# Performance work log

Hardware: AMD Instinct MI355X
Metric: run time of the kernel (lower is better)

Reference implementation:

```python
import jax, jax.numpy as jnp
import numpy as np

DIM = 1024
EXPAND = 2
HEAD_DIM = 64
D_STATE = 128
N_GROUPS = 1
D_CONV = 4
D_INNER = DIM * EXPAND            # 2048
N_HEADS = D_INNER // HEAD_DIM     # 32
CONV_DIM = D_INNER + 2 * N_GROUPS * D_STATE  # 2304
D_IN_PROJ = 2 * D_INNER + 2 * N_GROUPS * D_STATE + N_HEADS  # 4384
SEQLEN = 4096
LN_EPS = 1e-5


def setup_inputs() -> dict:
    key = jax.random.key(0)
    ks = jax.random.split(key, 6)
    x = jax.random.normal(ks[0], (SEQLEN, DIM), dtype=jnp.float32)
    W_in = jax.random.normal(ks[1], (D_IN_PROJ, DIM), dtype=jnp.float32) * 0.02
    conv_w = jax.random.normal(ks[2], (CONV_DIM, 1, D_CONV), dtype=jnp.float32) * 0.2
    conv_b = jax.random.normal(ks[3], (CONV_DIM,), dtype=jnp.float32) * 0.02
    # dt_bias init per module: dt ~ exp(U*(log(dt_max)-log(dt_min))+log(dt_min)); inv-softplus
    u = jax.random.uniform(ks[4], (N_HEADS,))
    dt = jnp.exp(u * (np.log(0.1) - np.log(0.001)) + np.log(0.001))
    dt = jnp.clip(dt, 1e-4)
    dt_bias = dt + jnp.log(-jnp.expm1(-dt))
    A_log = jnp.log(jax.random.uniform(ks[5], (N_HEADS,), minval=1.0, maxval=16.0))
    D = jnp.ones((N_HEADS,), dtype=jnp.float32)
    ln_w = jnp.ones((D_INNER,), dtype=jnp.float32)
    ln_b = jnp.zeros((D_INNER,), dtype=jnp.float32)
    W_out = jax.random.normal(jax.random.fold_in(key, 7), (DIM, D_INNER), dtype=jnp.float32) * 0.02
    return {"x": x, "W_in": W_in, "conv_w": conv_w, "conv_b": conv_b,
            "dt_bias": dt_bias, "A_log": A_log, "D": D,
            "ln_w": ln_w, "ln_b": ln_b, "W_out": W_out}


def _forward(x, W_in, conv_w, conv_b, dt_bias, A_log, D, ln_w, ln_b, W_out):
    L = x.shape[0]
    dtype = x.dtype
    A = -jnp.exp(A_log.astype(jnp.float32))  # (h,)
    zxbcdt = x @ W_in.T                       # (L, d_in_proj)
    z = zxbcdt[:, :D_INNER]                   # (L, d_inner)
    xbc = zxbcdt[:, D_INNER:D_INNER + CONV_DIM]
    dt = zxbcdt[:, -N_HEADS:]
    dt = jax.nn.softplus(dt.astype(jnp.float32) + dt_bias.astype(jnp.float32))  # (L, h)
    # depthwise 1D conv, SAME padding (module uses padding='SAME', then slices to L)
    xbc_c = jax.lax.conv_general_dilated(
        xbc.T[None],                          # (1, conv_dim, L)
        conv_w,                               # (conv_dim, 1, k)
        window_strides=(1,), padding='SAME',
        dimension_numbers=('NCH', 'OIH', 'NCH'),
        feature_group_count=CONV_DIM,
    )[0].T + conv_b                           # (L, conv_dim)
    xbc_s = jax.nn.silu(xbc_c)
    x_in = xbc_s[:, :D_INNER].reshape(L, N_HEADS, HEAD_DIM)      # (L, h, p)
    B = xbc_s[:, D_INNER:D_INNER + N_GROUPS * D_STATE]          # (L, n) with g=1
    C = xbc_s[:, D_INNER + N_GROUPS * D_STATE:]                 # (L, n)
    # non-causal linear attention (VSSD): y = C (B^T (x * dt * A)) + x * D
    dA = dt.astype(dtype) * A.astype(dtype)                     # (L, h)
    Vs = x_in * dA[..., None]                                   # (L, h, p)
    KV = jnp.einsum('ln,lhp->hnp', B, Vs)                       # (h, n, p)
    y = jnp.einsum('ln,hnp->lhp', C, KV) + x_in * D[None, :, None]
    y = y.reshape(L, D_INNER)
    # per-token LayerNorm, then multiplicative SiLU(z) gate
    mu = jnp.mean(y, axis=-1, keepdims=True)
    var = jnp.var(y, axis=-1, keepdims=True)
    yn = (y - mu) * jax.lax.rsqrt(var + LN_EPS) * ln_w + ln_b
    y = yn * jax.nn.silu(z)
    return y @ W_out.T                                          # (L, dim)


def reference(x, W_in, conv_w, conv_b, dt_bias, A_log, D, ln_w, ln_b, W_out):
    return _forward(x, W_in, conv_w, conv_b, dt_bias, A_log, D, ln_w, ln_b, W_out)
```

## Files before the change

kernel.cpp:

```cpp
#include <hip/hip_runtime.h>
#include <math.h>

#define SEQLEN    4096
#define DIM_IN    1024
#define D_INNER   2048
#define N_HEADS   32
#define D_STATE   128
#define CONV_DIM  2304
#define D_IN_PROJ 4384
#define PROJ_LD   4480
#define LN_EPS    1e-5f
#define KV_SPLIT  32

typedef __attribute__((ext_vector_type(8))) short bf16x8;
typedef __attribute__((ext_vector_type(4))) float f32x4;
typedef __attribute__((ext_vector_type(8))) short short8;

__device__ __forceinline__ ushort f2bf(float f) {
    union { float f; unsigned u; } v; v.f = f;
    unsigned u = v.u + 0x7FFFu + ((v.u >> 16) & 1u);
    return (ushort)(u >> 16);
}
__device__ __forceinline__ float bf2f(ushort h) {
    union { unsigned u; float f; } v; v.u = ((unsigned)h) << 16;
    return v.f;
}

__device__ __forceinline__ void gload16(const void* g, void* l) {
    __builtin_amdgcn_global_load_lds(
        (const __attribute__((address_space(1))) void*)g,
        (__attribute__((address_space(3))) void*)l, 16, 0, 0);
}

#define XB_GROUPS   (SEQLEN * DIM_IN / 8)
#define WIN_GROUPS  (PROJ_LD * DIM_IN / 8)
#define WOUT_GROUPS (DIM_IN * D_INNER / 8)
__global__ __launch_bounds__(256)
void cvt_all(const float* __restrict__ x, const float* __restrict__ W_in,
             const float* __restrict__ W_out,
             ushort* __restrict__ xb, ushort* __restrict__ Winb,
             ushort* __restrict__ Woutb) {
    int i = blockIdx.x * 256 + threadIdx.x;
    const float* src;
    ushort* dst;
    int gi;
    if (i < XB_GROUPS) {
        src = x; dst = xb; gi = i;
    } else if (i < XB_GROUPS + WIN_GROUPS) {
        gi = i - XB_GROUPS;
        int row = (gi * 8) >> 10;
        if (row >= D_IN_PROJ) {
            *reinterpret_cast<short8*>(&Winb[(size_t)gi * 8]) = (short8){0,0,0,0,0,0,0,0};
            return;
        }
        src = W_in; dst = Winb;
    } else if (i < XB_GROUPS + WIN_GROUPS + WOUT_GROUPS) {
        gi = i - (XB_GROUPS + WIN_GROUPS);
        src = W_out; dst = Woutb;
    } else return;
    float4 v0 = reinterpret_cast<const float4*>(src)[gi * 2];
    float4 v1 = reinterpret_cast<const float4*>(src)[gi * 2 + 1];
    short8 r;
    r[0] = f2bf(v0.x); r[1] = f2bf(v0.y); r[2] = f2bf(v0.z); r[3] = f2bf(v0.w);
    r[4] = f2bf(v1.x); r[5] = f2bf(v1.y); r[6] = f2bf(v1.z); r[7] = f2bf(v1.w);
    *reinterpret_cast<short8*>(&dst[(size_t)gi * 8]) = r;
}
#define CVT_TOTAL (XB_GROUPS + WIN_GROUPS + WOUT_GROUPS)

template<int NT, int NTB>
__global__ __launch_bounds__(512, 4)
void gemm_bf16_big(const ushort* __restrict__ A, int lda,
                   const ushort* __restrict__ B, int ldb,
                   ushort* __restrict__ Cout, int ldc) {
    __shared__ __align__(16) ushort S[3][12288];

    const int nwg = gridDim.x;
    const int wg  = blockIdx.x;
    const int swz = (wg & 7) * (nwg >> 3) + (wg >> 3);
    const int m0 = (swz / NTB) * 256;
    const int n0 = (swz % NTB) * 128;

    const int tid  = threadIdx.x;
    const int wave = tid >> 6;
    const int lane = tid & 63;
    const int wr = wave >> 1;
    const int wc = wave & 1;
    const int r16 = lane & 15;
    const int kg  = lane >> 4;
    const int pkg = kg ^ ((r16 >> 1) & 3);

    f32x4 acc[4][4];
    #pragma unroll
    for (int i = 0; i < 4; ++i)
        #pragma unroll
        for (int j = 0; j < 4; ++j) acc[i][j] = (f32x4){0.f, 0.f, 0.f, 0.f};

    const int srow = lane >> 2;
    const int scol = ((lane & 3) ^ ((lane >> 3) & 3)) * 8;
    const ushort* gsrc[3];
    #pragma unroll
    for (int i = 0; i < 3; ++i) {
        int c = wave * 3 + i;
        gsrc[i] = (c < 16)
            ? A + (size_t)(m0 + c * 16 + srow) * lda + scol
            : B + (size_t)(n0 + (c - 16) * 16 + srow) * ldb + scol;
    }

#define STAGE_BIG(T, BUF)                                            \
    {                                                                \
        const int _k = (T) * 32;                                     \
        _Pragma("unroll")                                            \
        for (int i = 0; i < 3; ++i)                                  \
            gload16(gsrc[i] + _k, &S[BUF][(wave * 3 + i) * 512]);    \
    }

    STAGE_BIG(0, 0)
    STAGE_BIG(1, 1)

    int rb = 0;
    for (int t = 0; t < NT; ++t) {
        __builtin_amdgcn_sched_barrier(0);
        if (t + 1 < NT) {
            asm volatile("s_waitcnt vmcnt(3)" ::: "memory");
        } else {
            asm volatile("s_waitcnt vmcnt(0)" ::: "memory");
        }
        __builtin_amdgcn_s_barrier();
        __builtin_amdgcn_sched_barrier(0);

        if (t + 2 < NT) {
            int sb = rb + 2; if (sb >= 3) sb -= 3;
            STAGE_BIG(t + 2, sb)
        }

        const ushort* sp = &S[rb][0];
        bf16x8 a4[4], b4[4];
        #pragma unroll
        for (int ni = 0; ni < 4; ++ni)
            b4[ni] = *reinterpret_cast<const bf16x8*>(
                &sp[8192 + (wc * 64 + ni * 16 + r16) * 32 + pkg * 8]);
        #pragma unroll
        for (int mi = 0; mi < 4; ++mi)
            a4[mi] = *reinterpret_cast<const bf16x8*>(
                &sp[(wr * 64 + mi * 16 + r16) * 32 + pkg * 8]);
        __builtin_amdgcn_s_setprio(1);
        #pragma unroll
        for (int mi = 0; mi < 4; ++mi)
            #pragma unroll
            for (int ni = 0; ni < 4; ++ni)
                acc[mi][ni] = __builtin_amdgcn_mfma_f32_16x16x32_bf16(
                    a4[mi], b4[ni], acc[mi][ni], 0, 0, 0);
        __builtin_amdgcn_s_setprio(0);

        rb = (rb == 2) ? 0 : rb + 1;
    }
#undef STAGE_BIG

    ushort* EP = &S[0][0];
    __syncthreads();
    #pragma unroll
    for (int mi = 0; mi < 4; ++mi)
        #pragma unroll
        for (int ni = 0; ni < 4; ++ni)
            #pragma unroll
            for (int r = 0; r < 4; ++r)
                EP[(wr * 64 + mi * 16 + kg * 4 + r) * 136 + wc * 64 + ni * 16 + r16] =
                    f2bf(acc[mi][ni][r]);
    __syncthreads();
    #pragma unroll
    for (int i = 0; i < 8; ++i) {
        int idx = tid + 512 * i;
        int row = idx >> 4;
        int cb  = idx & 15;
        bf16x8 v = *reinterpret_cast<const bf16x8*>(&EP[row * 136 + cb * 8]);
        *reinterpret_cast<bf16x8*>(
            &Cout[(size_t)(m0 + row) * ldc + n0 + cb * 8]) = v;
    }
}

template<int BN, int NT, int OUTBF, int NTB>
__global__ __launch_bounds__(256)
void gemm_bf16_pipe(const ushort* __restrict__ A, int lda,
                    const ushort* __restrict__ B, int ldb,
                    void* __restrict__ Cout, int ldc) {
    constexpr int NI  = BN / 32;
    constexpr int BNP = BN + 8;
    __shared__ __align__(16) ushort As[3][128 * 32];
    __shared__ __align__(16) ushort Bs[3][BN * 32];

    const int nwg = gridDim.x;
    const int wg  = blockIdx.x;
    const int swz = (wg & 7) * (nwg >> 3) + (wg >> 3);
    const int m0 = (swz / NTB) * 128;
    const int n0 = (swz % NTB) * BN;

    const int tid  = threadIdx.x;
    const int wave = tid >> 6;
    const int lane = tid & 63;
    const int wm = (wave & 1) * 64;
    const int wn = (wave >> 1) * (BN / 2);
    const int r16 = lane & 15;
    const int kg  = lane >> 4;
    const int pkg = kg ^ ((r16 >> 1) & 3);

    f32x4 acc[4][NI];
    #pragma unroll
    for (int i = 0; i < 4; ++i)
        #pragma unroll
        for (int j = 0; j < NI; ++j) acc[i][j] = (f32x4){0.f, 0.f, 0.f, 0.f};

    const int srow = lane >> 2;
    const int scol = ((lane & 3) ^ ((lane >> 3) & 3)) * 8;
    const int ca0 = wave * 2, ca1 = wave * 2 + 1;
    const ushort* gA0 = A + (size_t)(m0 + ca0 * 16 + srow) * lda + scol;
    const ushort* gA1 = A + (size_t)(m0 + ca1 * 16 + srow) * lda + scol;
    const ushort* gB0;
    const ushort* gB1 = nullptr;
    int cb0, cb1 = 0;
    if constexpr (BN == 128) {
        cb0 = wave * 2; cb1 = wave * 2 + 1;
        gB0 = B + (size_t)(n0 + cb0 * 16 + srow) * ldb + scol;
        gB1 = B + (size_t)(n0 + cb1 * 16 + srow) * ldb + scol;
    } else {
        cb0 = wave;
        gB0 = B + (size_t)(n0 + cb0 * 16 + srow) * ldb + scol;
    }

#define STAGE_STEP(T, BUF)                                          \
    {                                                               \
        const int _k = (T) * 32;                                    \
        gload16(gA0 + _k, &As[BUF][ca0 * 512]);                     \
        gload16(gA1 + _k, &As[BUF][ca1 * 512]);                     \
        gload16(gB0 + _k, &Bs[BUF][cb0 * 512]);                     \
        if constexpr (BN == 128) gload16(gB1 + _k, &Bs[BUF][cb1 * 512]); \
    }

    STAGE_STEP(0, 0)
    STAGE_STEP(1, 1)

    int rb = 0;
    for (int t = 0; t < NT; ++t) {
        __builtin_amdgcn_sched_barrier(0);
        if (t + 1 < NT) {
            if constexpr (BN == 128) asm volatile("s_waitcnt vmcnt(4)" ::: "memory");
            else                     asm volatile("s_waitcnt vmcnt(3)" ::: "memory");
        } else {
            asm volatile("s_waitcnt vmcnt(0)" ::: "memory");
        }
        __builtin_amdgcn_s_barrier();
        __builtin_amdgcn_sched_barrier(0);

        if (t + 2 < NT) {
            int sb = rb + 2; if (sb >= 3) sb -= 3;
            STAGE_STEP(t + 2, sb)
        }

        const ushort* ab = &As[rb][0];
        const ushort* bb = &Bs[rb][0];
        bf16x8 a[4], b[NI];
        #pragma unroll
        for (int mi = 0; mi < 4; ++mi)
            a[mi] = *reinterpret_cast<const bf16x8*>(&ab[(wm + mi * 16 + r16) * 32 + pkg * 8]);
        #pragma unroll
        for (int ni = 0; ni < NI; ++ni)
            b[ni] = *reinterpret_cast<const bf16x8*>(&bb[(wn + ni * 16 + r16) * 32 + pkg * 8]);

        __builtin_amdgcn_s_setprio(1);
        #pragma unroll
        for (int mi = 0; mi < 4; ++mi)
            #pragma unroll
            for (int ni = 0; ni < NI; ++ni)
                acc[mi][ni] = __builtin_amdgcn_mfma_f32_16x16x32_bf16(a[mi], b[ni], acc[mi][ni], 0, 0, 0);
        __builtin_amdgcn_s_setprio(0);

        rb = (rb == 2) ? 0 : rb + 1;
    }
#undef STAGE_STEP

    if constexpr (OUTBF) {
        ushort* EP = &As[0][0];
        ushort* outp = (ushort*)Cout;
        __syncthreads();
        #pragma unroll
        for (int half = 0; half < 2; ++half) {
            if ((wave & 1) == half) {
                #pragma unroll
                for (int mi = 0; mi < 4; ++mi)
                    #pragma unroll
                    for (int ni = 0; ni < NI; ++ni)
                        #pragma unroll
                        for (int r = 0; r < 4; ++r)
                            EP[(mi * 16 + kg * 4 + r) * BNP + wn + ni * 16 + r16] =
                                f2bf(acc[mi][ni][r]);
            }
            __syncthreads();
            #pragma unroll
            for (int i = 0; i < BN / 32; ++i) {
                int idx = tid + 256 * i;
                int row = idx / (BN / 8);
                int cb  = idx % (BN / 8);
                bf16x8 v = *reinterpret_cast<const bf16x8*>(&EP[row * BNP + cb * 8]);
                *reinterpret_cast<bf16x8*>(
                    &outp[(size_t)(m0 + half * 64 + row) * ldc + n0 + cb * 8]) = v;
            }
            __syncthreads();
        }
    } else {
        float* outp = (float*)Cout;
        #pragma unroll
        for (int mi = 0; mi < 4; ++mi)
            #pragma unroll
            for (int ni = 0; ni < NI; ++ni)
                #pragma unroll
                for (int r = 0; r < 4; ++r) {
                    int row = m0 + wm + mi * 16 + kg * 4 + r;
                    int col = n0 + wn + ni * 16 + r16;
                    outp[(size_t)row * ldc + col] = acc[mi][ni][r];
                }
    }
}

__global__ __launch_bounds__(256)
void conv_silu_kernel(const ushort* __restrict__ zxb,
                      const float* __restrict__ conv_w,
                      const float* __restrict__ conv_b,
                      const float* __restrict__ dt_bias,
                      const float* __restrict__ A_log,
                      ushort* __restrict__ xbcs,
                      float* __restrict__ dA) {
    const int l = blockIdx.x;
    const ushort* base = zxb + (size_t)l * PROJ_LD + D_INNER;
    const short8 zero8 = (short8){0,0,0,0,0,0,0,0};
    for (int g = threadIdx.x; g < CONV_DIM / 8; g += 256) {
        const int c = g * 8;
        short8 xm = (l >= 1)
            ? *reinterpret_cast<const short8*>(base + c - PROJ_LD) : zero8;
        short8 x0 = *reinterpret_cast<const short8*>(base + c);
        short8 xp = (l + 1 < SEQLEN)
            ? *reinterpret_cast<const short8*>(base + c + PROJ_LD) : zero8;
        short8 xq = (l + 2 < SEQLEN)
            ? *reinterpret_cast<const short8*>(base + c + 2 * PROJ_LD) : zero8;
        float4 bia0 = *reinterpret_cast<const float4*>(&conv_b[c]);
        float4 bia1 = *reinterpret_cast<const float4*>(&conv_b[c + 4]);
        short8 o;
        #pragma unroll
        for (int j = 0; j < 8; ++j) {
            float4 w = *reinterpret_cast<const float4*>(&conv_w[(c + j) * 4]);
            float acc = (j < 4 ? (&bia0.x)[j] : (&bia1.x)[j - 4]);
            acc += w.x * bf2f((ushort)xm[j]);
            acc += w.y * bf2f((ushort)x0[j]);
            acc += w.z * bf2f((ushort)xp[j]);
            acc += w.w * bf2f((ushort)xq[j]);
            float s = acc / (1.0f + expf(-acc));
            o[j] = f2bf(s);
        }
        *reinterpret_cast<short8*>(&xbcs[(size_t)l * CONV_DIM + c]) = o;
    }
    if (threadIdx.x < N_HEADS) {
        int h = threadIdx.x;
        float v = bf2f(zxb[(size_t)l * PROJ_LD + (D_IN_PROJ - N_HEADS) + h]) + dt_bias[h];
        float sp = (v > 20.0f) ? v : log1pf(expf(v));
        dA[l * N_HEADS + h] = sp * (-expf(A_log[h]));
    }
}

__global__ __launch_bounds__(256)
void kv_kernel(const ushort* __restrict__ xbcs,
               const float* __restrict__ dA,
               float* __restrict__ KVp) {
    __shared__ float Vs[16][132];
    __shared__ float Bsm[16][132];
    const int hp0 = blockIdx.x * 128;
    const int lc0 = blockIdx.y * (SEQLEN / KV_SPLIT);
    const int tid = threadIdx.x;
    const int ty = tid >> 4, tx = tid & 15;
    float acc[8][8];
    #pragma unroll
    for (int i = 0; i < 8; ++i)
        #pragma unroll
        for (int j = 0; j < 8; ++j) acc[i][j] = 0.0f;

    for (int ls = 0; ls < SEQLEN / KV_SPLIT; ls += 16) {
        {
            int lrow = tid >> 4;
            int p8   = (tid & 15) * 8;
            int l = lc0 + ls + lrow;
            short8 v = *reinterpret_cast<const short8*>(
                &xbcs[(size_t)l * CONV_DIM + hp0 + p8]);
            float a = dA[l * N_HEADS + ((hp0 + p8) >> 6)];
            #pragma unroll
            for (int j = 0; j < 8; ++j) Vs[lrow][p8 + j] = bf2f((ushort)v[j]) * a;
            short8 b = *reinterpret_cast<const short8*>(
                &xbcs[(size_t)l * CONV_DIM + D_INNER + p8]);
            #pragma unroll
            for (int j = 0; j < 8; ++j) Bsm[lrow][p8 + j] = bf2f((ushort)b[j]);
        }
        __syncthreads();
        #pragma unroll
        for (int k = 0; k < 16; ++k) {
            float a[8], b[8];
            *reinterpret_cast<float4*>(&a[0]) = *reinterpret_cast<const float4*>(&Vs[k][ty * 8]);
            *reinterpret_cast<float4*>(&a[4]) = *reinterpret_cast<const float4*>(&Vs[k][ty * 8 + 4]);
            *reinterpret_cast<float4*>(&b[0]) = *reinterpret_cast<const float4*>(&Bsm[k][tx * 8]);
            *reinterpret_cast<float4*>(&b[4]) = *reinterpret_cast<const float4*>(&Bsm[k][tx * 8 + 4]);
            #pragma unroll
            for (int i = 0; i < 8; ++i)
                #pragma unroll
                for (int j = 0; j < 8; ++j)
                    acc[i][j] = fmaf(a[i], b[j], acc[i][j]);
        }
        __syncthreads();
    }
    float* dst = KVp + (size_t)blockIdx.y * (D_INNER * D_STATE);
    #pragma unroll
    for (int i = 0; i < 8; ++i) {
        int hp = hp0 + ty * 8 + i;
        #pragma unroll
        for (int j = 0; j < 8; j += 4) {
            float4 v = make_float4(acc[i][j], acc[i][j+1], acc[i][j+2], acc[i][j+3]);
            *reinterpret_cast<float4*>(&dst[(size_t)hp * D_STATE + tx * 8 + j]) = v;
        }
    }
}

__global__ __launch_bounds__(256)
void kv_reduce(const float* __restrict__ KVp, ushort* __restrict__ KVTb) {
    int i = blockIdx.x * 256 + threadIdx.x;
    float4 s = make_float4(0.f, 0.f, 0.f, 0.f);
    #pragma unroll
    for (int c = 0; c < KV_SPLIT; ++c) {
        float4 v = reinterpret_cast<const float4*>(KVp + (size_t)c * (D_INNER * D_STATE))[i];
        s.x += v.x; s.y += v.y; s.z += v.z; s.w += v.w;
    }
    ushort4 o;
    o.x = f2bf(s.x); o.y = f2bf(s.y); o.z = f2bf(s.z); o.w = f2bf(s.w);
    *reinterpret_cast<ushort4*>(&KVTb[i * 4]) = o;
}

__global__ __launch_bounds__(256)
void ln_gate_kernel(const ushort* __restrict__ y1b,
                    const ushort* __restrict__ xbcs,
                    const ushort* __restrict__ zxb,
                    const float* __restrict__ Dp,
                    const float* __restrict__ ln_w,
                    const float* __restrict__ ln_b,
                    ushort* __restrict__ yb) {
    const int l = blockIdx.x;
    const int tid = threadIdx.x;
    const int c = tid * 8;
    float y[8], z[8];
    float sum = 0.f, sumsq = 0.f;
    {
        short8 v  = *reinterpret_cast<const short8*>(&y1b[(size_t)l * D_INNER + c]);
        short8 xi = *reinterpret_cast<const short8*>(&xbcs[(size_t)l * CONV_DIM + c]);
        short8 zz = *reinterpret_cast<const short8*>(&zxb[(size_t)l * PROJ_LD + c]);
        float d = Dp[c >> 6];
        #pragma unroll
        for (int j = 0; j < 8; ++j) {
            float yv = bf2f((ushort)v[j]) + bf2f((ushort)xi[j]) * d;
            y[j] = yv;
            z[j] = bf2f((ushort)zz[j]);
            sum += yv;
            sumsq += yv * yv;
        }
    }
    #pragma unroll
    for (int off = 32; off > 0; off >>= 1) {
        sum   += __shfl_down(sum, off);
        sumsq += __shfl_down(sumsq, off);
    }
    __shared__ float red[8];
    int wid = tid >> 6;
    if ((tid & 63) == 0) { red[wid] = sum; red[4 + wid] = sumsq; }
    __syncthreads();
    sum   = red[0] + red[1] + red[2] + red[3];
    sumsq = red[4] + red[5] + red[6] + red[7];
    float mu  = sum * (1.0f / D_INNER);
    float var = sumsq * (1.0f / D_INNER) - mu * mu;
    float rs  = rsqrtf(var + LN_EPS);
    short8 o;
    #pragma unroll
    for (int j = 0; j < 8; ++j) {
        float yn = (y[j] - mu) * rs * ln_w[c + j] + ln_b[c + j];
        float g  = z[j] / (1.0f + expf(-z[j]));
        o[j] = f2bf(yn * g);
    }
    *reinterpret_cast<short8*>(&yb[(size_t)l * D_INNER + c]) = o;
}

extern "C" void kernel_launch(void* const* d_in, const int* in_sizes, int n_in,
                              void* d_out, int out_size, void* d_ws, size_t ws_size,
                              hipStream_t stream) {
    const float* x       = (const float*)d_in[0];
    const float* W_in    = (const float*)d_in[1];
    const float* conv_w  = (const float*)d_in[2];
    const float* conv_b  = (const float*)d_in[3];
    const float* dt_bias = (const float*)d_in[4];
    const float* A_log   = (const float*)d_in[5];
    const float* Dp      = (const float*)d_in[6];
    const float* ln_w    = (const float*)d_in[7];
    const float* ln_b    = (const float*)d_in[8];
    const float* W_out   = (const float*)d_in[9];
    float* out = (float*)d_out;

    char* ws = (char*)d_ws;
    ushort* zxb   = (ushort*)ws;
    ushort* xbcs  = (ushort*)(ws +  36700160);
    ushort* y1b   = (ushort*)(ws +  55574528);
    ushort* yb    = (ushort*)(ws +  72351744);
    float*  KVp   = (float*)(ws +  89128960);
    float*  dA    = (float*)(ws + 122683392);
    ushort* KVTb  = (ushort*)(ws + 123207680);
    ushort* Woutb = (ushort*)(ws + 123731968);
    ushort* xb    = (ushort*)(ws + 127926272);
    ushort* Winb  = (ushort*)(ws + 136314880);

    cvt_all<<<(CVT_TOTAL + 255) / 256, 256, 0, stream>>>(x, W_in, W_out, xb, Winb, Woutb);

    gemm_bf16_big<32, 35><<<16 * (PROJ_LD / 128), 512, 0, stream>>>(
        xb, DIM_IN, Winb, DIM_IN, zxb, PROJ_LD);

    conv_silu_kernel<<<SEQLEN, 256, 0, stream>>>(zxb, conv_w, conv_b, dt_bias, A_log,
                                                 xbcs, dA);

    kv_kernel<<<dim3(16, KV_SPLIT), 256, 0, stream>>>(xbcs, dA, KVp);
    kv_reduce<<<(D_INNER * D_STATE / 4) / 256, 256, 0, stream>>>(KVp, KVTb);

    gemm_bf16_pipe<128, 4, 1, 16><<<(D_INNER / 128) * 32, 256, 0, stream>>>(
        xbcs + (D_INNER + D_STATE), CONV_DIM, KVTb, D_STATE, y1b, D_INNER);

    ln_gate_kernel<<<SEQLEN, 256, 0, stream>>>(y1b, xbcs, zxb, Dp, ln_w, ln_b, yb);

    gemm_bf16_pipe<64, 64, 0, 16><<<(DIM_IN / 64) * 32, 256, 0, stream>>>(
        yb, D_INNER, Woutb, D_INNER, out, DIM_IN);
}
```

Baseline: 189.1 us.

## Double K-tile depth of input-projection GEMM to 64 with new LDS swizzle

The big input-projection GEMM now stages K=64 per pipeline step instead of 32. It halves the iteration count and the barriers per tile and doubles the MFMA work between syncs. The LDS layout uses a new 8-way XOR swizzle over 64-element rows, and each wave issues six 16-byte global-to-LDS loads per stage. LDS use doubles to about 144KB across three buffers and launch_bounds drops to 2 blocks/CU, which may reduce occupancy.

```diff
diff --git a/kernel.cpp b/kernel.cpp
--- a/kernel.cpp
+++ b/kernel.cpp
@@ -68,11 +68,11 @@
 #define CVT_TOTAL (XB_GROUPS + WIN_GROUPS + WOUT_GROUPS)
 
 template<int NT, int NTB>
-__global__ __launch_bounds__(512, 4)
+__global__ __launch_bounds__(512, 2)
 void gemm_bf16_big(const ushort* __restrict__ A, int lda,
                    const ushort* __restrict__ B, int ldb,
                    ushort* __restrict__ Cout, int ldc) {
-    __shared__ __align__(16) ushort S[3][12288];
+    __shared__ __align__(16) ushort S[3][24576];
 
     const int nwg = gridDim.x;
     const int wg  = blockIdx.x;
@@ -87,7 +87,7 @@
     const int wc = wave & 1;
     const int r16 = lane & 15;
     const int kg  = lane >> 4;
-    const int pkg = kg ^ ((r16 >> 1) & 3);
+    const int sx  = r16 & 7;
 
     f32x4 acc[4][4];
     #pragma unroll
@@ -95,23 +95,28 @@
         #pragma unroll
         for (int j = 0; j < 4; ++j) acc[i][j] = (f32x4){0.f, 0.f, 0.f, 0.f};
 
-    const int srow = lane >> 2;
-    const int scol = ((lane & 3) ^ ((lane >> 3) & 3)) * 8;
-    const ushort* gsrc[3];
-    #pragma unroll
-    for (int i = 0; i < 3; ++i) {
-        int c = wave * 3 + i;
-        gsrc[i] = (c < 16)
-            ? A + (size_t)(m0 + c * 16 + srow) * lda + scol
-            : B + (size_t)(n0 + (c - 16) * 16 + srow) * ldb + scol;
+    const int lr = lane >> 3;
+    const int lslot = ((lane & 7) ^ lr) * 8;
+    const ushort* gsrc[6];
+    int ldsoff[6];
+    #pragma unroll
+    for (int i = 0; i < 6; ++i) {
+        int c = wave * 6 + i;
+        if (c < 32) {
+            gsrc[i] = A + (size_t)(m0 + 8 * c + lr) * lda + lslot;
+            ldsoff[i] = c * 512;
+        } else {
+            gsrc[i] = B + (size_t)(n0 + 8 * (c - 32) + lr) * ldb + lslot;
+            ldsoff[i] = 16384 + (c - 32) * 512;
+        }
     }
 
 #define STAGE_BIG(T, BUF)                                            \
     {                                                                \
-        const int _k = (T) * 32;                                     \
+        const int _k = (T) * 64;                                     \
         _Pragma("unroll")                                            \
-        for (int i = 0; i < 3; ++i)                                  \
-            gload16(gsrc[i] + _k, &S[BUF][(wave * 3 + i) * 512]);    \
+        for (int i = 0; i < 6; ++i)                                  \
+            gload16(gsrc[i] + _k, &S[BUF][ldsoff[i]]);               \
     }
 
     STAGE_BIG(0, 0)
@@ -121,7 +126,7 @@
     for (int t = 0; t < NT; ++t) {
         __builtin_amdgcn_sched_barrier(0);
         if (t + 1 < NT) {
-            asm volatile("s_waitcnt vmcnt(3)" ::: "memory");
+            asm volatile("s_waitcnt vmcnt(6)" ::: "memory");
         } else {
             asm volatile("s_waitcnt vmcnt(0)" ::: "memory");
         }
@@ -134,22 +139,28 @@
         }
 
         const ushort* sp = &S[rb][0];
-        bf16x8 a4[4], b4[4];
+        bf16x8 a4[4][2], b4[4][2];
         #pragma unroll
         for (int ni = 0; ni < 4; ++ni)
-            b4[ni] = *reinterpret_cast<const bf16x8*>(
-                &sp[8192 + (wc * 64 + ni * 16 + r16) * 32 + pkg * 8]);
+            #pragma unroll
+            for (int s = 0; s < 2; ++s)
+                b4[ni][s] = *reinterpret_cast<const bf16x8*>(
+                    &sp[16384 + (wc * 64 + ni * 16 + r16) * 64 + (((s * 4 + kg) ^ sx) * 8)]);
         #pragma unroll
         for (int mi = 0; mi < 4; ++mi)
-            a4[mi] = *reinterpret_cast<const bf16x8*>(
-                &sp[(wr * 64 + mi * 16 + r16) * 32 + pkg * 8]);
+            #pragma unroll
+            for (int s = 0; s < 2; ++s)
+                a4[mi][s] = *reinterpret_cast<const bf16x8*>(
+                    &sp[(wr * 64 + mi * 16 + r16) * 64 + (((s * 4 + kg) ^ sx) * 8)]);
         __builtin_amdgcn_s_setprio(1);
         #pragma unroll
         for (int mi = 0; mi < 4; ++mi)
             #pragma unroll
             for (int ni = 0; ni < 4; ++ni)
-                acc[mi][ni] = __builtin_amdgcn_mfma_f32_16x16x32_bf16(
-                    a4[mi], b4[ni], acc[mi][ni], 0, 0, 0);
+                #pragma unroll
+                for (int s = 0; s < 2; ++s)
+                    acc[mi][ni] = __builtin_amdgcn_mfma_f32_16x16x32_bf16(
+                        a4[mi][s], b4[ni][s], acc[mi][ni], 0, 0, 0);
         __builtin_amdgcn_s_setprio(0);
 
         rb = (rb == 2) ? 0 : rb + 1;
@@ -517,7 +528,7 @@
 
     cvt_all<<<(CVT_TOTAL + 255) / 256, 256, 0, stream>>>(x, W_in, W_out, xb, Winb, Woutb);
 
-    gemm_bf16_big<32, 35><<<16 * (PROJ_LD / 128), 512, 0, stream>>>(
+    gemm_bf16_big<16, 35><<<16 * (PROJ_LD / 128), 512, 0, stream>>>(
         xb, DIM_IN, Winb, DIM_IN, zxb, PROJ_LD);
 
     conv_silu_kernel<<<SEQLEN, 256, 0, stream>>>(zxb, conv_w, conv_b, dt_bias, A_log,
```

New measurement: 190.9 us. Within noise of the previous version (+1.0%).
